# Kernel tuning notes

Measured on AMD Instinct MI355X. Metric: run time of the kernel, lower is better.

The kernel has to match this reference:

```python
import jax, jax.numpy as jnp
import numpy as np

B, S, D = 2, 2048, 1024
H = 16
HD = D // H  # 64
EPS = 1e-6
ROPE_BASE = 10000.0


def _rms_norm(x, w, eps=EPS):
    # torch nn.RMSNorm over last dim
    var = jnp.mean(jnp.square(x), axis=-1, keepdims=True)
    return x * jax.lax.rsqrt(var + eps) * w


def _rope_tables(seq_len, head_dim, base=ROPE_BASE):
    inv_freq = 1.0 / (base ** (jnp.arange(0, head_dim, 2, dtype=jnp.float32) / head_dim))
    t = jnp.arange(seq_len, dtype=jnp.float32)
    freqs = t[:, None] * inv_freq[None, :]            # [S, HD/2]
    emb = jnp.concatenate([freqs, freqs], axis=-1)    # [S, HD]
    return jnp.cos(emb), jnp.sin(emb)


def _rotate_half(x):
    x1, x2 = jnp.split(x, 2, axis=-1)
    return jnp.concatenate([-x2, x1], axis=-1)


def _apply_rope(x, cos, sin):
    # x: [B, H, S, HD]; cos/sin: [S, HD]
    return x * cos[None, None] + _rotate_half(x) * sin[None, None]


def setup_inputs() -> dict:
    key = jax.random.key(0)
    ks = jax.random.split(key, 8)
    scale = 1.0 / np.sqrt(D)
    return {
        "x": jax.random.normal(ks[0], (B, S, D), dtype=jnp.float32),
        "wq": jax.random.normal(ks[1], (D, D), dtype=jnp.float32) * scale,
        "wk": jax.random.normal(ks[2], (D, D), dtype=jnp.float32) * scale,
        "wv": jax.random.normal(ks[3], (D, D), dtype=jnp.float32) * scale,
        "wo": jax.random.normal(ks[4], (D, D), dtype=jnp.float32) * scale,
        "q_norm_w": jnp.ones((HD,), dtype=jnp.float32),
        "k_norm_w": jnp.ones((HD,), dtype=jnp.float32),
        "sink_logit": jnp.zeros((H,), dtype=jnp.float32),
    }


def reference(x, wq, wk, wv, wo, q_norm_w, k_norm_w, sink_logit):
    b, s, _ = x.shape
    # QKV projections (nn.Linear, no bias): y = x @ W^T
    q = jnp.einsum("bsd,od->bso", x, wq).reshape(b, s, H, HD)
    k = jnp.einsum("bsd,od->bso", x, wk).reshape(b, s, H, HD)
    v = jnp.einsum("bsd,od->bso", x, wv).reshape(b, s, H, HD)
    # QK RMSNorm (per head_dim)
    q = _rms_norm(q, q_norm_w)
    k = _rms_norm(k, k_norm_w)
    # [B, H, S, HD]
    q = q.transpose(0, 2, 1, 3)
    k = k.transpose(0, 2, 1, 3)
    v = v.transpose(0, 2, 1, 3)
    # full-head RoPE
    cos, sin = _rope_tables(s, HD)
    q = _apply_rope(q, cos, sin)
    k = _apply_rope(k, cos, sin)
    # manual attention with causal mask and sink softmax
    scale = HD ** -0.5
    scores = jnp.einsum("bhqd,bhkd->bhqk", q, k) * scale  # [B,H,S,S]
    causal = jnp.tril(jnp.ones((s, s), dtype=bool))
    scores = jnp.where(causal[None, None], scores, -jnp.inf)
    # sink-augmented softmax in fp32: append per-head sink logit, softmax, drop sink column
    sink = jnp.broadcast_to(sink_logit.astype(jnp.float32)[None, :, None, None], (b, H, s, 1))
    aug = jnp.concatenate([scores.astype(jnp.float32), sink], axis=-1)
    weights = jax.nn.softmax(aug, axis=-1)[..., :s].astype(scores.dtype)
    out = jnp.einsum("bhqk,bhkd->bhqd", weights, v)
    out = out.transpose(0, 2, 1, 3).reshape(b, s, D)
    return jnp.einsum("bsd,od->bso", out, wo)
```

## Files before the change

### kernel.cpp

```cpp
#include <hip/hip_runtime.h>

#define Bb 2
#define Ss 2048
#define Dd 1024
#define Hh 16
#define HDd 64
#define BS (Bb * Ss)

typedef __attribute__((ext_vector_type(8))) __bf16 bf16x8;
typedef __attribute__((ext_vector_type(8))) unsigned short u16x8;
typedef __attribute__((ext_vector_type(4))) float f32x4;

__device__ __forceinline__ unsigned short f2bf(float f) {
  union { float f; unsigned u; } v; v.f = f;
  unsigned r = v.u + 0x7fffu + ((v.u >> 16) & 1u);
  return (unsigned short)(r >> 16);
}
__device__ __forceinline__ unsigned short f2bf_fast(float f) {
  union { float f; unsigned u; } v; v.f = f;
  return (unsigned short)((v.u + 0x8000u) >> 16);
}

__device__ __forceinline__ void gl_lds16(const void* g, void* l) {
  __builtin_amdgcn_global_load_lds(
      (const __attribute__((address_space(1))) void*)g,
      (__attribute__((address_space(3))) void*)l, 16, 0, 0);
}

__global__ __launch_bounds__(256) void cast_all(
    const float4* __restrict__ x, const float4* __restrict__ wq,
    const float4* __restrict__ wk, const float4* __restrict__ wv,
    const float4* __restrict__ wo, ushort4* __restrict__ xb,
    ushort4* __restrict__ wqkvb, ushort4* __restrict__ wob,
    float* __restrict__ ct, float* __restrict__ st) {
  int i = blockIdx.x * 256 + threadIdx.x;
  const int NX4 = BS * Dd / 4;
  const int NW4 = Dd * Dd / 4;
  const float4* src;
  ushort4* dst;
  int idx;
  if (i < NX4) { src = x; dst = xb; idx = i; }
  else if ((i -= NX4) < NW4) { src = wq; dst = wqkvb; idx = i; }
  else if ((i -= NW4) < NW4) { src = wk; dst = wqkvb + NW4; idx = i; }
  else if ((i -= NW4) < NW4) { src = wv; dst = wqkvb + 2 * NW4; idx = i; }
  else if ((i -= NW4) < NW4) { src = wo; dst = wob; idx = i; }
  else if ((i -= NW4) < Ss * 32) {
    int s = i >> 5, jj = i & 31;
    float freq = __powf(10000.0f, -(float)jj * (1.0f / 32.0f));
    float cs, sn;
    sincosf((float)s * freq, &sn, &cs);
    ct[i] = cs; st[i] = sn;
    return;
  } else return;
  float4 v = src[idx];
  ushort4 o;
  o.x = f2bf(v.x); o.y = f2bf(v.y); o.z = f2bf(v.z); o.w = f2bf(v.w);
  dst[idx] = o;
}

__global__ __launch_bounds__(256) void gemm_qkv(
    const unsigned short* __restrict__ A, const unsigned short* __restrict__ Bw,
    const float* __restrict__ qw, const float* __restrict__ kw,
    const float* __restrict__ ct, const float* __restrict__ st,
    unsigned short* __restrict__ Qb, unsigned short* __restrict__ Kb,
    unsigned short* __restrict__ Vt) {
  __shared__ __align__(16) unsigned short As[128 * 32];
  __shared__ __align__(16) unsigned short Bs[128 * 32];
  const int K = Dd, tid = threadIdx.x;
  const int lane = tid & 63;
  const int quad = lane >> 4;
  const int l16 = lane & 15;
  const int wave = tid >> 6;
  const int wm = (wave >> 1) * 64;
  const int wn = (wave & 1) * 64;
  const int tile_m = blockIdx.y * 128;
  const int tile_n = blockIdx.x * 128;

  const int off0 = tid * 16;
  const int off1 = 4096 + tid * 16;
  const int r0 = tid >> 2, r1 = r0 + 64;
  const int sch = (((tid & 3) ^ ((tid >> 3) & 3)) << 3);
  const int xg = ((quad ^ ((l16 >> 1) & 3)) << 3);

  const unsigned short* Ag0 = A + (size_t)(tile_m + r0) * K + sch;
  const unsigned short* Ag1 = A + (size_t)(tile_m + r1) * K + sch;
  const unsigned short* Bg0 = Bw + (size_t)(tile_n + r0) * K + sch;
  const unsigned short* Bg1 = Bw + (size_t)(tile_n + r1) * K + sch;

  f32x4 zero = {0.f, 0.f, 0.f, 0.f};
  f32x4 acc[4][4];
#pragma unroll
  for (int mi = 0; mi < 4; ++mi)
#pragma unroll
    for (int ni = 0; ni < 4; ++ni) acc[mi][ni] = zero;

  for (int k0 = 0; k0 < K; k0 += 32) {
    gl_lds16(Ag0 + k0, (char*)As + off0);
    gl_lds16(Ag1 + k0, (char*)As + off1);
    gl_lds16(Bg0 + k0, (char*)Bs + off0);
    gl_lds16(Bg1 + k0, (char*)Bs + off1);
    __syncthreads();
    bf16x8 af[4], bfv[4];
#pragma unroll
    for (int mi = 0; mi < 4; ++mi)
      af[mi] = *(const bf16x8*)&As[(wm + mi * 16 + l16) * 32 + xg];
#pragma unroll
    for (int ni = 0; ni < 4; ++ni)
      bfv[ni] = *(const bf16x8*)&Bs[(wn + ni * 16 + l16) * 32 + xg];
#pragma unroll
    for (int mi = 0; mi < 4; ++mi)
#pragma unroll
      for (int ni = 0; ni < 4; ++ni)
        acc[mi][ni] = __builtin_amdgcn_mfma_f32_16x16x32_bf16(
            af[mi], bfv[ni], acc[mi][ni], 0, 0, 0);
    __syncthreads();
  }

  const int type = blockIdx.x >> 3;
  const int h = (((blockIdx.x & 7) << 7) + wn) >> 6;
  const int bb = tile_m >> 11;
  const size_t bh = (size_t)bb * Hh + h;

  if (type == 2) {
#pragma unroll
    for (int mi = 0; mi < 4; ++mi) {
      int s0 = (tile_m + wm + mi * 16 + quad * 4) & (Ss - 1);
#pragma unroll
      for (int ni = 0; ni < 4; ++ni) {
        int d = ni * 16 + l16;
        ushort4 pv;
        pv.x = f2bf(acc[mi][ni][0]);
        pv.y = f2bf(acc[mi][ni][1]);
        pv.z = f2bf(acc[mi][ni][2]);
        pv.w = f2bf(acc[mi][ni][3]);
        *(ushort4*)&Vt[(bh * HDd + d) * Ss + s0] = pv;
      }
    }
  } else {
    const float* wnp = type ? kw : qw;
    unsigned short* Ob = type ? Kb : Qb;
    const float fscale = type ? 1.0f : 0.125f * 1.44269504f;
    float w0[4];
#pragma unroll
    for (int ni = 0; ni < 4; ++ni) w0[ni] = wnp[ni * 16 + l16];
#pragma unroll
    for (int mi = 0; mi < 4; ++mi) {
#pragma unroll
      for (int r = 0; r < 4; ++r) {
        int s = (tile_m + wm + mi * 16 + quad * 4 + r) & (Ss - 1);
        float ss2 = 0.f;
#pragma unroll
        for (int ni = 0; ni < 4; ++ni) ss2 += acc[mi][ni][r] * acc[mi][ni][r];
        ss2 += __shfl_xor(ss2, 1, 64);
        ss2 += __shfl_xor(ss2, 2, 64);
        ss2 += __shfl_xor(ss2, 4, 64);
        ss2 += __shfl_xor(ss2, 8, 64);
        float rr = rsqrtf(ss2 * (1.0f / 64.0f) + 1e-6f) * fscale;
        float c0 = ct[s * 32 + l16], c1 = ct[s * 32 + 16 + l16];
        float sn0 = st[s * 32 + l16], sn1 = st[s * 32 + 16 + l16];
#pragma unroll
        for (int ni = 0; ni < 4; ++ni) {
          float vn = acc[mi][ni][r] * rr * w0[ni];
          float vp = acc[mi][ni ^ 2][r] * rr * w0[ni ^ 2];
          float cs_ = (ni & 1) ? c1 : c0;
          float sn_ = (ni & 1) ? sn1 : sn0;
          float sg = (ni < 2) ? -1.0f : 1.0f;
          Ob[(bh * Ss + s) * HDd + ni * 16 + l16] = f2bf(vn * cs_ + sg * vp * sn_);
        }
      }
    }
  }
}

__global__ __launch_bounds__(256) void gemm_bt2(
    const unsigned short* __restrict__ A, const unsigned short* __restrict__ Bw,
    float* __restrict__ C, int M, int N, int K) {
  __shared__ __align__(16) unsigned short As[128 * 32];
  __shared__ __align__(16) unsigned short Bs[64 * 32];
  const int tid = threadIdx.x;
  const int lane = tid & 63;
  const int quad = lane >> 4;
  const int l16 = lane & 15;
  const int wave = tid >> 6;
  const int wm = (wave >> 1) * 64;
  const int wn = (wave & 1) * 32;
  const int tile_m = blockIdx.y * 128;
  const int tile_n = blockIdx.x * 64;

  const int off0 = tid * 16;
  const int off1 = 4096 + tid * 16;
  const int r0 = tid >> 2, r1 = r0 + 64;
  const int sch = (((tid & 3) ^ ((tid >> 3) & 3)) << 3);
  const int xg = ((quad ^ ((l16 >> 1) & 3)) << 3);

  const unsigned short* Ag0 = A + (size_t)(tile_m + r0) * K + sch;
  const unsigned short* Ag1 = A + (size_t)(tile_m + r1) * K + sch;
  const unsigned short* Bg0 = Bw + (size_t)(tile_n + r0) * K + sch;

  f32x4 zero = {0.f, 0.f, 0.f, 0.f};
  f32x4 acc[4][2];
#pragma unroll
  for (int mi = 0; mi < 4; ++mi)
#pragma unroll
    for (int ni = 0; ni < 2; ++ni) acc[mi][ni] = zero;

  for (int k0 = 0; k0 < K; k0 += 32) {
    gl_lds16(Ag0 + k0, (char*)As + off0);
    gl_lds16(Ag1 + k0, (char*)As + off1);
    gl_lds16(Bg0 + k0, (char*)Bs + off0);
    __syncthreads();
    bf16x8 af[4], bfv[2];
#pragma unroll
    for (int mi = 0; mi < 4; ++mi)
      af[mi] = *(const bf16x8*)&As[(wm + mi * 16 + l16) * 32 + xg];
#pragma unroll
    for (int ni = 0; ni < 2; ++ni)
      bfv[ni] = *(const bf16x8*)&Bs[(wn + ni * 16 + l16) * 32 + xg];
#pragma unroll
    for (int mi = 0; mi < 4; ++mi)
#pragma unroll
      for (int ni = 0; ni < 2; ++ni)
        acc[mi][ni] = __builtin_amdgcn_mfma_f32_16x16x32_bf16(
            af[mi], bfv[ni], acc[mi][ni], 0, 0, 0);
    __syncthreads();
  }

#pragma unroll
  for (int mi = 0; mi < 4; ++mi) {
#pragma unroll
    for (int ni = 0; ni < 2; ++ni) {
      int col = tile_n + wn + ni * 16 + l16;
#pragma unroll
      for (int r = 0; r < 4; ++r) {
        int row = tile_m + wm + mi * 16 + quad * 4 + r;
        C[(size_t)row * N + col] = acc[mi][ni][r];
      }
    }
  }
}

__global__ __launch_bounds__(256) void flash(
    const unsigned short* __restrict__ Qb, const unsigned short* __restrict__ Kb,
    const unsigned short* __restrict__ Vt, const float* __restrict__ sink,
    unsigned short* __restrict__ Ob) {
  __shared__ __align__(16) unsigned short Qs[64 * 64];
  __shared__ __align__(16) unsigned short Ks[2][64 * 64];
  __shared__ __align__(16) unsigned short Vs[3][64 * 64];
  __shared__ __align__(16) unsigned short Ps[4][16 * 72];

  int tid = threadIdx.x, lane = tid & 63, wave = tid >> 6;
  int quad = lane >> 4, l16 = lane & 15;
  int bx = blockIdx.x;
  int h = blockIdx.y, b = blockIdx.z;

  const unsigned short* Qg = Qb + ((size_t)(b * Hh + h) * Ss) * HDd;
  const unsigned short* Kg = Kb + ((size_t)(b * Hh + h) * Ss) * HDd;
  const unsigned short* Vg = Vt + ((size_t)(b * Hh + h) * HDd) * Ss;

  int off0 = tid * 16, off1 = 4096 + tid * 16;
  int sr0 = tid >> 3, sr1 = sr0 + 32;
  int sch = ((tid & 7) ^ (sr0 & 7)) * 8;
  int x0 = ((quad ^ (l16 & 7)) * 8);
  int x1 = x0 ^ 32;

  float sk = sink[h];
  f32x4 zero = {0.f, 0.f, 0.f, 0.f};

  bf16x8 ones;
  {
    u16x8 t;
#pragma unroll
    for (int i = 0; i < 8; ++i) t[i] = 0x3F80;
    ones = *(bf16x8*)&t;
  }

#pragma unroll 1
  for (int pass = 0; pass < 2; ++pass) {
    int qt = pass ? bx : 31 - bx;
    int q0 = qt * 64;
    int myq = q0 + wave * 16 + l16;

    __syncthreads();
    gl_lds16(Qg + (size_t)(q0 + sr0) * 64 + sch, (char*)Qs + off0);
    gl_lds16(Qg + (size_t)(q0 + sr1) * 64 + sch, (char*)Qs + off1);
    gl_lds16(Kg + (size_t)sr0 * 64 + sch, (char*)Ks[0] + off0);
    gl_lds16(Kg + (size_t)sr1 * 64 + sch, (char*)Ks[0] + off1);
    gl_lds16(Vg + (size_t)sr0 * Ss + sch, (char*)Vs[0] + off0);
    gl_lds16(Vg + (size_t)sr1 * Ss + sch, (char*)Vs[0] + off1);

    f32x4 Oacc[4], lacc = zero;
#pragma unroll
    for (int ni = 0; ni < 4; ++ni) Oacc[ni] = zero;

    __syncthreads();
    bf16x8 aq0 = *(const bf16x8*)&Qs[(wave * 16 + l16) * 64 + x0];
    bf16x8 aq1 = *(const bf16x8*)&Qs[(wave * 16 + l16) * 64 + x1];
    if (qt >= 1) {
      gl_lds16(Kg + (size_t)(64 + sr0) * 64 + sch, (char*)Ks[1] + off0);
      gl_lds16(Kg + (size_t)(64 + sr1) * 64 + sch, (char*)Ks[1] + off1);
      gl_lds16(Vg + (size_t)sr0 * Ss + 64 + sch, (char*)Vs[1] + off0);
      gl_lds16(Vg + (size_t)sr1 * Ss + 64 + sch, (char*)Vs[1] + off1);
    }

    f32x4 sc[4];
#pragma unroll
    for (int ni = 0; ni < 4; ++ni) {
      bf16x8 bk0 = *(const bf16x8*)&Ks[0][(ni * 16 + l16) * 64 + x0];
      bf16x8 bk1 = *(const bf16x8*)&Ks[0][(ni * 16 + l16) * 64 + x1];
      sc[ni] = __builtin_amdgcn_mfma_f32_16x16x32_bf16(bk0, aq0, zero, 0, 0, 0);
      sc[ni] = __builtin_amdgcn_mfma_f32_16x16x32_bf16(bk1, aq1, sc[ni], 0, 0, 0);
    }
    if (qt == 0) {
#pragma unroll
      for (int ni = 0; ni < 4; ++ni)
#pragma unroll
        for (int r = 0; r < 4; ++r)
          if (ni * 16 + quad * 4 + r > myq - q0) sc[ni][r] = -1.0e38f;
    }

    for (int kt = 0; kt <= qt; ++kt) {
      bool last = (kt == qt);
      if (!last) __syncthreads();
      if (kt + 2 <= qt) {
        int vb = (kt + 2) % 3, kb = kt & 1;
        gl_lds16(Kg + (size_t)((kt + 2) * 64 + sr0) * 64 + sch, (char*)Ks[kb] + off0);
        gl_lds16(Kg + (size_t)((kt + 2) * 64 + sr1) * 64 + sch, (char*)Ks[kb] + off1);
        gl_lds16(Vg + (size_t)sr0 * Ss + (kt + 2) * 64 + sch, (char*)Vs[vb] + off0);
        gl_lds16(Vg + (size_t)sr1 * Ss + (kt + 2) * 64 + sch, (char*)Vs[vb] + off1);
      }

#pragma unroll
      for (int ni = 0; ni < 4; ++ni) {
        ushort4 pk;
        pk.x = f2bf_fast(exp2f(sc[ni][0]));
        pk.y = f2bf_fast(exp2f(sc[ni][1]));
        pk.z = f2bf_fast(exp2f(sc[ni][2]));
        pk.w = f2bf_fast(exp2f(sc[ni][3]));
        *(ushort4*)&Ps[wave][l16 * 72 + ni * 16 + quad * 4] = pk;
      }

      f32x4 scn[4];
      if (!last) {
        const unsigned short* Kt = Ks[(kt + 1) & 1];
#pragma unroll
        for (int ni = 0; ni < 4; ++ni) {
          bf16x8 bk0 = *(const bf16x8*)&Kt[(ni * 16 + l16) * 64 + x0];
          bf16x8 bk1 = *(const bf16x8*)&Kt[(ni * 16 + l16) * 64 + x1];
          scn[ni] = __builtin_amdgcn_mfma_f32_16x16x32_bf16(bk0, aq0, zero, 0, 0, 0);
          scn[ni] = __builtin_amdgcn_mfma_f32_16x16x32_bf16(bk1, aq1, scn[ni], 0, 0, 0);
        }
        if (kt + 1 == qt) {
#pragma unroll
          for (int ni = 0; ni < 4; ++ni)
#pragma unroll
            for (int r = 0; r < 4; ++r)
              if ((kt + 1) * 64 + ni * 16 + quad * 4 + r > myq) scn[ni][r] = -1.0e38f;
        }
      }

      asm volatile("s_waitcnt lgkmcnt(0)" ::: "memory");
      bf16x8 ap0 = *(const bf16x8*)&Ps[wave][l16 * 72 + quad * 8];
      bf16x8 ap1 = *(const bf16x8*)&Ps[wave][l16 * 72 + 32 + quad * 8];

      const unsigned short* Vtile = Vs[kt % 3];
#pragma unroll
      for (int ni = 0; ni < 4; ++ni) {
        bf16x8 bv0 = *(const bf16x8*)&Vtile[(ni * 16 + l16) * 64 + x0];
        bf16x8 bv1 = *(const bf16x8*)&Vtile[(ni * 16 + l16) * 64 + x1];
        Oacc[ni] = __builtin_amdgcn_mfma_f32_16x16x32_bf16(bv0, ap0, Oacc[ni], 0, 0, 0);
        Oacc[ni] = __builtin_amdgcn_mfma_f32_16x16x32_bf16(bv1, ap1, Oacc[ni], 0, 0, 0);
      }
      lacc = __builtin_amdgcn_mfma_f32_16x16x32_bf16(ones, ap0, lacc, 0, 0, 0);
      lacc = __builtin_amdgcn_mfma_f32_16x16x32_bf16(ones, ap1, lacc, 0, 0, 0);

      if (!last) {
#pragma unroll
        for (int ni = 0; ni < 4; ++ni) sc[ni] = scn[ni];
      }
    }

    float inv = 1.0f / (lacc[0] + exp2f(sk * 1.44269504f));
#pragma unroll
    for (int ni = 0; ni < 4; ++ni) {
      ushort4 ov;
      ov.x = f2bf(Oacc[ni][0] * inv);
      ov.y = f2bf(Oacc[ni][1] * inv);
      ov.z = f2bf(Oacc[ni][2] * inv);
      ov.w = f2bf(Oacc[ni][3] * inv);
      *(ushort4*)&Ob[((size_t)b * Ss + myq) * Dd + h * 64 + ni * 16 + quad * 4] = ov;
    }
  }
}

extern "C" void kernel_launch(void* const* d_in, const int* in_sizes, int n_in,
                              void* d_out, int out_size, void* d_ws, size_t ws_size,
                              hipStream_t stream) {
  const float* x  = (const float*)d_in[0];
  const float* wq = (const float*)d_in[1];
  const float* wk = (const float*)d_in[2];
  const float* wv = (const float*)d_in[3];
  const float* wo = (const float*)d_in[4];
  const float* qw = (const float*)d_in[5];
  const float* kw = (const float*)d_in[6];
  const float* sk = (const float*)d_in[7];

  char* ws = (char*)d_ws;
  const size_t MB = 1ull << 20;
  unsigned short* xb    = (unsigned short*)(ws + 0);
  unsigned short* attnb = (unsigned short*)(ws + 0);
  unsigned short* wqkvb = (unsigned short*)(ws + 8 * MB);
  unsigned short* wob   = (unsigned short*)(ws + 14 * MB);
  float*          ct    = (float*)(ws + 16 * MB);
  float*          st    = (float*)(ws + 17 * MB);
  unsigned short* Qb    = (unsigned short*)(ws + 40 * MB);
  unsigned short* Kb    = (unsigned short*)(ws + 48 * MB);
  unsigned short* Vt    = (unsigned short*)(ws + 56 * MB);

  cast_all<<<8448, 256, 0, stream>>>(
      (const float4*)x, (const float4*)wq, (const float4*)wk, (const float4*)wv,
      (const float4*)wo, (ushort4*)xb, (ushort4*)wqkvb, (ushort4*)wob, ct, st);
  gemm_qkv<<<dim3(24, 32), 256, 0, stream>>>(xb, wqkvb, qw, kw, ct, st, Qb, Kb, Vt);
  flash<<<dim3(16, Hh, Bb), 256, 0, stream>>>(Qb, Kb, Vt, sk, attnb);
  gemm_bt2<<<dim3(16, 32), 256, 0, stream>>>(attnb, wob, (float*)d_out, BS, Dd, Dd);
}
```

Before: 201.5 us.

## Share K/V tiles across two adjacent query tiles in 512-thread flash blocks

The flash kernel now uses 512-thread blocks where each half of the block processes one of two adjacent 64-row query tiles, so each K/V tile loaded into LDS serves 128 query rows. The Q buffer is reused as per-wave P scratch with an XOR-swizzled layout in place of padded rows. This halves the grid and roughly halves K/V global traffic per query row. In exchange, the lower half idles on the final diagonal iteration, and each block holds more waves and registers, which may reduce occupancy.

```diff
diff --git a/kernel.cpp b/kernel.cpp
--- a/kernel.cpp
+++ b/kernel.cpp
@@ -239,16 +239,16 @@
   }
 }
 
-__global__ __launch_bounds__(256) void flash(
+__global__ __launch_bounds__(512) void flash(
     const unsigned short* __restrict__ Qb, const unsigned short* __restrict__ Kb,
     const unsigned short* __restrict__ Vt, const float* __restrict__ sink,
     unsigned short* __restrict__ Ob) {
-  __shared__ __align__(16) unsigned short Qs[64 * 64];
+  __shared__ __align__(16) unsigned short QP[8192];
   __shared__ __align__(16) unsigned short Ks[2][64 * 64];
   __shared__ __align__(16) unsigned short Vs[3][64 * 64];
-  __shared__ __align__(16) unsigned short Ps[4][16 * 72];
 
   int tid = threadIdx.x, lane = tid & 63, wave = tid >> 6;
+  int half = wave >> 2, wl = wave & 3;
   int quad = lane >> 4, l16 = lane & 15;
   int bx = blockIdx.x;
   int h = blockIdx.y, b = blockIdx.z;
@@ -257,12 +257,13 @@
   const unsigned short* Kg = Kb + ((size_t)(b * Hh + h) * Ss) * HDd;
   const unsigned short* Vg = Vt + ((size_t)(b * Hh + h) * HDd) * Ss;
 
-  int off0 = tid * 16, off1 = 4096 + tid * 16;
-  int sr0 = tid >> 3, sr1 = sr0 + 32;
-  int sch = ((tid & 7) ^ (sr0 & 7)) * 8;
+  int off = tid * 16;
+  int sr = tid >> 3;
+  int sch = ((tid & 7) ^ (sr & 7)) * 8;
   int x0 = ((quad ^ (l16 & 7)) * 8);
   int x1 = x0 ^ 32;
 
+  unsigned short* Pw = QP + wave * 1024;
   float sk = sink[h];
   f32x4 zero = {0.f, 0.f, 0.f, 0.f};
 
@@ -276,31 +277,25 @@
 
 #pragma unroll 1
   for (int pass = 0; pass < 2; ++pass) {
-    int qt = pass ? bx : 31 - bx;
-    int q0 = qt * 64;
-    int myq = q0 + wave * 16 + l16;
-
-    __syncthreads();
-    gl_lds16(Qg + (size_t)(q0 + sr0) * 64 + sch, (char*)Qs + off0);
-    gl_lds16(Qg + (size_t)(q0 + sr1) * 64 + sch, (char*)Qs + off1);
-    gl_lds16(Kg + (size_t)sr0 * 64 + sch, (char*)Ks[0] + off0);
-    gl_lds16(Kg + (size_t)sr1 * 64 + sch, (char*)Ks[0] + off1);
-    gl_lds16(Vg + (size_t)sr0 * Ss + sch, (char*)Vs[0] + off0);
-    gl_lds16(Vg + (size_t)sr1 * Ss + sch, (char*)Vs[0] + off1);
+    int qtBig = pass ? (2 * bx + 1) : (31 - 2 * bx);
+    int qth = qtBig - half;
+    int myq = qth * 64 + wl * 16 + l16;
+
+    __syncthreads();
+    gl_lds16(Qg + (size_t)(qtBig * 64 + sr) * 64 + sch, (char*)QP + off);
+    gl_lds16(Qg + (size_t)((qtBig - 1) * 64 + sr) * 64 + sch, (char*)QP + 8192 + off);
+    gl_lds16(Kg + (size_t)sr * 64 + sch, (char*)Ks[0] + off);
+    gl_lds16(Vg + (size_t)sr * Ss + sch, (char*)Vs[0] + off);
 
     f32x4 Oacc[4], lacc = zero;
 #pragma unroll
     for (int ni = 0; ni < 4; ++ni) Oacc[ni] = zero;
 
     __syncthreads();
-    bf16x8 aq0 = *(const bf16x8*)&Qs[(wave * 16 + l16) * 64 + x0];
-    bf16x8 aq1 = *(const bf16x8*)&Qs[(wave * 16 + l16) * 64 + x1];
-    if (qt >= 1) {
-      gl_lds16(Kg + (size_t)(64 + sr0) * 64 + sch, (char*)Ks[1] + off0);
-      gl_lds16(Kg + (size_t)(64 + sr1) * 64 + sch, (char*)Ks[1] + off1);
-      gl_lds16(Vg + (size_t)sr0 * Ss + 64 + sch, (char*)Vs[1] + off0);
-      gl_lds16(Vg + (size_t)sr1 * Ss + 64 + sch, (char*)Vs[1] + off1);
-    }
+    bf16x8 aq0 = *(const bf16x8*)&QP[(half * 64 + wl * 16 + l16) * 64 + x0];
+    bf16x8 aq1 = *(const bf16x8*)&QP[(half * 64 + wl * 16 + l16) * 64 + x1];
+    gl_lds16(Kg + (size_t)(64 + sr) * 64 + sch, (char*)Ks[1] + off);
+    gl_lds16(Vg + (size_t)sr * Ss + 64 + sch, (char*)Vs[1] + off);
 
     f32x4 sc[4];
 #pragma unroll
@@ -310,37 +305,39 @@
       sc[ni] = __builtin_amdgcn_mfma_f32_16x16x32_bf16(bk0, aq0, zero, 0, 0, 0);
       sc[ni] = __builtin_amdgcn_mfma_f32_16x16x32_bf16(bk1, aq1, sc[ni], 0, 0, 0);
     }
-    if (qt == 0) {
+    if (qth == 0) {
 #pragma unroll
       for (int ni = 0; ni < 4; ++ni)
 #pragma unroll
         for (int r = 0; r < 4; ++r)
-          if (ni * 16 + quad * 4 + r > myq - q0) sc[ni][r] = -1.0e38f;
-    }
-
-    for (int kt = 0; kt <= qt; ++kt) {
-      bool last = (kt == qt);
-      if (!last) __syncthreads();
-      if (kt + 2 <= qt) {
-        int vb = (kt + 2) % 3, kb = kt & 1;
-        gl_lds16(Kg + (size_t)((kt + 2) * 64 + sr0) * 64 + sch, (char*)Ks[kb] + off0);
-        gl_lds16(Kg + (size_t)((kt + 2) * 64 + sr1) * 64 + sch, (char*)Ks[kb] + off1);
-        gl_lds16(Vg + (size_t)sr0 * Ss + (kt + 2) * 64 + sch, (char*)Vs[vb] + off0);
-        gl_lds16(Vg + (size_t)sr1 * Ss + (kt + 2) * 64 + sch, (char*)Vs[vb] + off1);
-      }
-
-#pragma unroll
-      for (int ni = 0; ni < 4; ++ni) {
-        ushort4 pk;
-        pk.x = f2bf_fast(exp2f(sc[ni][0]));
-        pk.y = f2bf_fast(exp2f(sc[ni][1]));
-        pk.z = f2bf_fast(exp2f(sc[ni][2]));
-        pk.w = f2bf_fast(exp2f(sc[ni][3]));
-        *(ushort4*)&Ps[wave][l16 * 72 + ni * 16 + quad * 4] = pk;
+          if (ni * 16 + quad * 4 + r > myq) sc[ni][r] = -1.0e38f;
+    }
+
+    for (int kt = 0; kt <= qtBig; ++kt) {
+      bool lastBig = (kt == qtBig);
+      bool active = (kt <= qth);
+      bool pipeN = (kt + 1 <= qth);
+      if (!lastBig) __syncthreads();
+      if (kt + 2 <= qtBig) {
+        gl_lds16(Kg + (size_t)((kt + 2) * 64 + sr) * 64 + sch, (char*)Ks[kt & 1] + off);
+        gl_lds16(Vg + (size_t)sr * Ss + (kt + 2) * 64 + sch, (char*)Vs[(kt + 2) % 3] + off);
+      }
+
+      if (active) {
+#pragma unroll
+        for (int ni = 0; ni < 4; ++ni) {
+          ushort4 pk;
+          pk.x = f2bf_fast(exp2f(sc[ni][0]));
+          pk.y = f2bf_fast(exp2f(sc[ni][1]));
+          pk.z = f2bf_fast(exp2f(sc[ni][2]));
+          pk.w = f2bf_fast(exp2f(sc[ni][3]));
+          int slot = ((ni * 2 + (quad >> 1)) ^ (l16 & 7)) * 8 + (quad & 1) * 4;
+          *(ushort4*)&Pw[l16 * 64 + slot] = pk;
+        }
       }
 
       f32x4 scn[4];
-      if (!last) {
+      if (pipeN) {
         const unsigned short* Kt = Ks[(kt + 1) & 1];
 #pragma unroll
         for (int ni = 0; ni < 4; ++ni) {
@@ -349,7 +346,7 @@
           scn[ni] = __builtin_amdgcn_mfma_f32_16x16x32_bf16(bk0, aq0, zero, 0, 0, 0);
           scn[ni] = __builtin_amdgcn_mfma_f32_16x16x32_bf16(bk1, aq1, scn[ni], 0, 0, 0);
         }
-        if (kt + 1 == qt) {
+        if (kt + 1 == qth) {
 #pragma unroll
           for (int ni = 0; ni < 4; ++ni)
 #pragma unroll
@@ -358,22 +355,24 @@
         }
       }
 
-      asm volatile("s_waitcnt lgkmcnt(0)" ::: "memory");
-      bf16x8 ap0 = *(const bf16x8*)&Ps[wave][l16 * 72 + quad * 8];
-      bf16x8 ap1 = *(const bf16x8*)&Ps[wave][l16 * 72 + 32 + quad * 8];
-
-      const unsigned short* Vtile = Vs[kt % 3];
-#pragma unroll
-      for (int ni = 0; ni < 4; ++ni) {
-        bf16x8 bv0 = *(const bf16x8*)&Vtile[(ni * 16 + l16) * 64 + x0];
-        bf16x8 bv1 = *(const bf16x8*)&Vtile[(ni * 16 + l16) * 64 + x1];
-        Oacc[ni] = __builtin_amdgcn_mfma_f32_16x16x32_bf16(bv0, ap0, Oacc[ni], 0, 0, 0);
-        Oacc[ni] = __builtin_amdgcn_mfma_f32_16x16x32_bf16(bv1, ap1, Oacc[ni], 0, 0, 0);
-      }
-      lacc = __builtin_amdgcn_mfma_f32_16x16x32_bf16(ones, ap0, lacc, 0, 0, 0);
-      lacc = __builtin_amdgcn_mfma_f32_16x16x32_bf16(ones, ap1, lacc, 0, 0, 0);
-
-      if (!last) {
+      if (active) {
+        asm volatile("s_waitcnt lgkmcnt(0)" ::: "memory");
+        bf16x8 ap0 = *(const bf16x8*)&Pw[l16 * 64 + x0];
+        bf16x8 ap1 = *(const bf16x8*)&Pw[l16 * 64 + x1];
+
+        const unsigned short* Vtile = Vs[kt % 3];
+#pragma unroll
+        for (int ni = 0; ni < 4; ++ni) {
+          bf16x8 bv0 = *(const bf16x8*)&Vtile[(ni * 16 + l16) * 64 + x0];
+          bf16x8 bv1 = *(const bf16x8*)&Vtile[(ni * 16 + l16) * 64 + x1];
+          Oacc[ni] = __builtin_amdgcn_mfma_f32_16x16x32_bf16(bv0, ap0, Oacc[ni], 0, 0, 0);
+          Oacc[ni] = __builtin_amdgcn_mfma_f32_16x16x32_bf16(bv1, ap1, Oacc[ni], 0, 0, 0);
+        }
+        lacc = __builtin_amdgcn_mfma_f32_16x16x32_bf16(ones, ap0, lacc, 0, 0, 0);
+        lacc = __builtin_amdgcn_mfma_f32_16x16x32_bf16(ones, ap1, lacc, 0, 0, 0);
+      }
+
+      if (pipeN) {
 #pragma unroll
         for (int ni = 0; ni < 4; ++ni) sc[ni] = scn[ni];
       }
@@ -420,6 +419,6 @@
       (const float4*)x, (const float4*)wq, (const float4*)wk, (const float4*)wv,
       (const float4*)wo, (ushort4*)xb, (ushort4*)wqkvb, (ushort4*)wob, ct, st);
   gemm_qkv<<<dim3(24, 32), 256, 0, stream>>>(xb, wqkvb, qw, kw, ct, st, Qb, Kb, Vt);
-  flash<<<dim3(16, Hh, Bb), 256, 0, stream>>>(Qb, Kb, Vt, sk, attnb);
+  flash<<<dim3(8, Hh, Bb), 512, 0, stream>>>(Qb, Kb, Vt, sk, attnb);
   gemm_bt2<<<dim3(16, 32), 256, 0, stream>>>(attnb, wob, (float*)d_out, BS, Dd, Dd);
 }
```

After: 202.8 us. About the same (+0.7%).
